# Optimization experiments

Measured on AMD Instinct MI355X. Metric: run time of the kernel, lower is better.

Reference implementation:

```python
import jax, jax.numpy as jnp
import numpy as np

W_EDGE, W_LAP, W_NORMAL, W_VEL = 0.5, 0.05, 0.01, 10.0


def _grid_mesh(g):
    ids = np.arange(g * g).reshape(g, g)
    tl, tr = ids[:-1, :-1].ravel(), ids[:-1, 1:].ravel()
    bl, br = ids[1:, :-1].ravel(), ids[1:, 1:].ravel()
    f1 = np.stack([tl, bl, br], 1)
    f2 = np.stack([tl, br, tr], 1)
    return np.concatenate([f1, f2], 0).astype(np.int64)  # [F,3]


def _topology(faces):
    # all directed edges with the opposite vertex of their face
    e = np.concatenate([faces[:, [0, 1]], faces[:, [1, 2]], faces[:, [2, 0]]], 0)
    opp = np.concatenate([faces[:, 2], faces[:, 0], faces[:, 1]], 0)
    key = np.sort(e, axis=1)
    uniq, inv = np.unique(key, axis=0, return_inverse=True)  # unique undirected edges
    counts = np.bincount(inv)
    order = np.argsort(inv, kind='stable')
    sel = counts[inv[order]] == 2
    idx2 = order[sel].reshape(-1, 2)  # the two face-slots of each interior edge
    ekey = key[idx2[:, 0]]
    pairs = np.stack([ekey[:, 0], ekey[:, 1], opp[idx2[:, 0]], opp[idx2[:, 1]]], 1)
    return uniq.astype(np.int64), pairs.astype(np.int64)


def setup_inputs() -> dict:
    key = jax.random.key(0)
    k1, k2 = jax.random.split(key)
    B, g = 2, 91
    N = g * g  # 8281
    faces = _grid_mesh(g)                 # [16200,3]
    edges, nc_pairs = _topology(faces)    # [24480,2], [24120,4]
    predictions = jax.random.normal(k1, (B, N, 3), dtype=jnp.float32)
    targets = jax.random.normal(k2, (B, N, 3), dtype=jnp.float32)
    return {
        'predictions': predictions,
        'targets': targets,
        'pred_faces': jnp.asarray(faces),
        'edges': jnp.asarray(edges),
        'nc_pairs': jnp.asarray(nc_pairs),
    }


def _chamfer(x, y):
    # pytorch3d chamfer_distance: squared dists, point mean both ways, batch mean
    xx = jnp.sum(x * x, -1)
    yy = jnp.sum(y * y, -1)
    d = xx[:, :, None] + yy[:, None, :] - 2.0 * jnp.einsum('bnd,bmd->bnm', x, y)
    d = jnp.maximum(d, 0.0)
    return jnp.mean(jnp.min(d, axis=2).mean(axis=1) + jnp.min(d, axis=1).mean(axis=1))


def _edge_loss(verts, edges):
    # mean over meshes of mean over edges of squared edge length (target len 0)
    ve = verts[:, edges]  # [B,E,2,3]
    l2 = jnp.sum((ve[:, :, 0] - ve[:, :, 1]) ** 2, -1)
    return l2.mean()


def _cot_laplacian_loss_one(verts, faces):
    # verts [N,3]; pytorch3d cot_laplacian + method='cot' smoothing
    fv = verts[faces]  # [F,3,3]
    v0, v1, v2 = fv[:, 0], fv[:, 1], fv[:, 2]
    A = jnp.linalg.norm(v1 - v2, axis=1)
    Bl = jnp.linalg.norm(v0 - v2, axis=1)
    C = jnp.linalg.norm(v0 - v1, axis=1)
    s = 0.5 * (A + Bl + C)
    area = jnp.sqrt(jnp.maximum(s * (s - A) * (s - Bl) * (s - C), 1e-12))
    A2, B2, C2 = A * A, Bl * Bl, C * C
    cota = (B2 + C2 - A2) / area
    cotb = (A2 + C2 - B2) / area
    cotc = (A2 + B2 - C2) / area
    cot = jnp.stack([cota, cotb, cotc], 1) / 4.0  # [F,3]
    ii = faces[:, jnp.array([1, 2, 0])]
    jj = faces[:, jnp.array([2, 0, 1])]
    i = jnp.concatenate([ii, jj], 0).ravel()
    j = jnp.concatenate([jj, ii], 0).ravel()
    w = jnp.concatenate([cot, cot], 0).ravel()
    N = verts.shape[0]
    Lx = jnp.zeros_like(verts).at[i].add(w[:, None] * verts[j])
    rowsum = jnp.zeros((N,), dtype=verts.dtype).at[i].add(w)
    norm_w = jnp.where(rowsum > 0, 1.0 / rowsum, 0.0)
    res = Lx * norm_w[:, None] - verts
    return jnp.linalg.norm(res, axis=1).mean()


def _normal_consistency_one(verts, pairs):
    # pairs [P,4] = (v0, v1, opp_a, opp_b) per interior edge
    p = verts[pairs]  # [P,4,3]
    e = p[:, 1] - p[:, 0]
    n0 = jnp.cross(e, p[:, 2] - p[:, 0])
    n1 = -jnp.cross(e, p[:, 3] - p[:, 0])
    eps = 1e-8
    cos = jnp.sum(n0 * n1, -1) / (
        jnp.maximum(jnp.linalg.norm(n0, axis=1), eps)
        * jnp.maximum(jnp.linalg.norm(n1, axis=1), eps)
    )
    return (1.0 - cos).mean()


def _forward(predictions, targets, pred_faces, edges, nc_pairs):
    loss_cham = _chamfer(predictions, targets)
    edge_l = _edge_loss(predictions, edges)
    lap_l = jax.vmap(lambda v: _cot_laplacian_loss_one(v, pred_faces))(predictions).mean()
    nc_l = jax.vmap(lambda v: _normal_consistency_one(v, nc_pairs))(predictions).mean()
    pred_shift = predictions[:, 1:, :] - predictions[:, :-1, :]
    tgt_shift = targets[:, 1:, :] - targets[:, :-1, :]
    vel_l = _chamfer(pred_shift, tgt_shift)
    return loss_cham + W_LAP * lap_l + W_NORMAL * nc_l + W_EDGE * edge_l + W_VEL * vel_l


def reference(predictions, targets, pred_faces, edges, nc_pairs):
    return _forward(predictions, targets, pred_faces, edges, nc_pairs)
```

## Files before the change

kernel.cpp:

```cpp
#include <hip/hip_runtime.h>


typedef unsigned int uint32;
typedef __attribute__((ext_vector_type(8)))  short bf16x8;
typedef __attribute__((ext_vector_type(16))) float f32x16;

#define W_EDGE   0.5f
#define W_LAP    0.05f
#define W_NORMAL 0.01f
#define W_VEL    10.0f
#define BIGF     3.0e38f
#define RSTRIDE  8320

__device__ __forceinline__ unsigned short f2bf(float f){
    uint32 b = __float_as_uint(f);
    b += 0x7FFFu + ((b >> 16) & 1u);
    return (unsigned short)(b >> 16);
}
__device__ __forceinline__ float bf2f(unsigned short h){
    return __uint_as_float(((uint32)h) << 16);
}

__device__ __forceinline__ float wave_sum(float v) {
#pragma unroll
    for (int o = 32; o > 0; o >>= 1) v += __shfl_down(v, o, 64);
    return v;
}

__global__ void bprep_k(const float* __restrict__ pred, const float* __restrict__ tgt,
                        int N, uint4* __restrict__ bfrag,
                        float* __restrict__ ws, int nzero)
{
    {
        uint32* w = (uint32*)ws;
        for (int i = blockIdx.x * blockDim.x + threadIdx.x; i < nzero;
             i += gridDim.x * blockDim.x)
            w[i] = 0u;
    }

    const int NT = (N + 31) >> 5;
    const int gt = blockIdx.x * 4 + (threadIdx.x >> 6);
    if (gt >= 8 * NT) return;
    const int c = gt / NT, t = gt - c * NT;
    const int dir = c >> 2, ds = (c >> 1) & 1, b = c & 1;
    const int Np = N - ds;
    const int l = threadIdx.x & 63;
    const int col = t * 32 + (l & 31);
    const float* __restrict__ yb = (dir ? pred : tgt) + (size_t)b * N * 3;
    float y0 = 0.f, y1 = 0.f, y2 = 0.f;
    const bool valid = col < Np;
    if (valid){
        if (ds){
            y0 = yb[(col+1)*3+0] - yb[col*3+0];
            y1 = yb[(col+1)*3+1] - yb[col*3+1];
            y2 = yb[(col+1)*3+2] - yb[col*3+2];
        } else {
            y0 = yb[col*3+0]; y1 = yb[col*3+1]; y2 = yb[col*3+2];
        }
    }
    const float yy = fmaf(y0,y0, fmaf(y1,y1, y2*y2));
    unsigned short yh0=f2bf(y0), yh1=f2bf(y1), yh2=f2bf(y2);
    unsigned short yl0=f2bf(y0-bf2f(yh0)), yl1=f2bf(y1-bf2f(yh1)), yl2=f2bf(y2-bf2f(yh2));
    unsigned short yyh, yyl;
    if (valid){ yyh = f2bf(yy); yyl = f2bf(yy - bf2f(yyh)); }
    else      { yyh = f2bf(BIGF); yyl = 0; }
    const short ONE = (short)0x3F80;
    bf16x8 Bu;
    if (l < 32){
        Bu[0]=(short)yh0; Bu[1]=(short)yh1; Bu[2]=(short)yh2;
        Bu[3]=(short)yh0; Bu[4]=(short)yh1; Bu[5]=(short)yh2;
        Bu[6]=(short)yl0; Bu[7]=(short)yl1;
    } else {
        Bu[0]=(short)yl2; Bu[1]=ONE; Bu[2]=ONE; Bu[3]=(short)yyh; Bu[4]=(short)yyl;
        Bu[5]=0; Bu[6]=0; Bu[7]=0;
    }
    bfrag[(size_t)(c * NT + t) * 64 + l] = __builtin_bit_cast(uint4, Bu);
}

__global__ __launch_bounds__(256)
void chamfer_mfma_k(const float* __restrict__ pred, const float* __restrict__ tgt,
                    int N, const uint4* __restrict__ bfrag,
                    float* __restrict__ rowpart)
{
    const int c = blockIdx.z;
    const int dir = c >> 2, ds = (c >> 1) & 1, b = c & 1;
    const int Np = N - ds;
    const int NT = (N + 31) >> 5;
    const int TC = (NT + 3) >> 2;
    const int t0 = blockIdx.y * TC;
    const int t1 = min(NT, t0 + TC);
    const int w = threadIdx.x >> 6, l = threadIdx.x & 63;
    const int h = l >> 5;
    const int grow = blockIdx.x * 128 + w * 32 + (l & 31);

    const float* __restrict__ xb = (dir ? tgt : pred) + (size_t)b * N * 3;
    float a0 = 0.f, a1 = 0.f, a2 = 0.f;
    const bool xvalid = grow < Np;
    if (xvalid){
        if (ds){
            a0 = xb[(grow+1)*3+0] - xb[grow*3+0];
            a1 = xb[(grow+1)*3+1] - xb[grow*3+1];
            a2 = xb[(grow+1)*3+2] - xb[grow*3+2];
        } else {
            a0 = xb[grow*3+0]; a1 = xb[grow*3+1]; a2 = xb[grow*3+2];
        }
    }
    const float xx = fmaf(a0,a0, fmaf(a1,a1, a2*a2));
    unsigned short xh0=f2bf(a0), xh1=f2bf(a1), xh2=f2bf(a2);
    unsigned short nxh0=f2bf(-2.f*bf2f(xh0)), nxh1=f2bf(-2.f*bf2f(xh1)), nxh2=f2bf(-2.f*bf2f(xh2));
    unsigned short nxl0=f2bf(-2.f*(a0-bf2f(xh0))), nxl1=f2bf(-2.f*(a1-bf2f(xh1))),
                   nxl2=f2bf(-2.f*(a2-bf2f(xh2)));
    unsigned short xxh=f2bf(xx), xxl=f2bf(xx-bf2f(xxh));
    const short ONE = (short)0x3F80;
    bf16x8 A;
    if (h == 0){
        A[0]=(short)nxh0; A[1]=(short)nxh1; A[2]=(short)nxh2;
        A[3]=(short)nxl0; A[4]=(short)nxl1; A[5]=(short)nxl2;
        A[6]=(short)nxh0; A[7]=(short)nxh1;
    } else {
        A[0]=(short)nxh2; A[1]=(short)xxh; A[2]=(short)xxl;
        A[3]=ONE; A[4]=ONE; A[5]=0; A[6]=0; A[7]=0;
    }

    f32x16 zacc;
#pragma unroll
    for (int r = 0; r < 16; ++r) zacc[r] = 0.f;
    float rm[16];
#pragma unroll
    for (int r = 0; r < 16; ++r) rm[r] = BIGF;

    const uint4* __restrict__ bfp = bfrag + (size_t)c * NT * 64 + l;

    const int ntile = t1 - t0;
    const int nb = ntile >> 3;

#define ONE_TILE(T)                                                         \
    {                                                                       \
        const f32x16 u = __builtin_amdgcn_mfma_f32_32x32x16_bf16(           \
            A, __builtin_bit_cast(bf16x8, T), zacc, 0, 0, 0);               \
        _Pragma("unroll")                                                   \
        for (int r = 0; r < 16; ++r) rm[r] = fminf(rm[r], u[r]);            \
    }                                                                       \
    __builtin_amdgcn_sched_barrier(0);

    int t = t0;
    for (int bt = 0; bt < nb; ++bt, t += 8){
        const uint4 T0 = bfp[(size_t)(t+0)*64];
        const uint4 T1 = bfp[(size_t)(t+1)*64];
        const uint4 T2 = bfp[(size_t)(t+2)*64];
        const uint4 T3 = bfp[(size_t)(t+3)*64];
        const uint4 T4 = bfp[(size_t)(t+4)*64];
        const uint4 T5 = bfp[(size_t)(t+5)*64];
        const uint4 T6 = bfp[(size_t)(t+6)*64];
        const uint4 T7 = bfp[(size_t)(t+7)*64];
        ONE_TILE(T0) ONE_TILE(T1) ONE_TILE(T2) ONE_TILE(T3)
        ONE_TILE(T4) ONE_TILE(T5) ONE_TILE(T6) ONE_TILE(T7)
    }
#undef ONE_TILE

    for (; t < t1; ++t){
        const bf16x8 T0 = __builtin_bit_cast(bf16x8, bfp[(size_t)t * 64]);
        const f32x16 u0 = __builtin_amdgcn_mfma_f32_32x32x16_bf16(A, T0, zacc, 0, 0, 0);
#pragma unroll
        for (int r = 0; r < 16; ++r) rm[r] = fminf(rm[r], u0[r]);
    }

#pragma unroll
    for (int r = 0; r < 16; ++r){
        float v = rm[r];
        v = fminf(v, __shfl_xor(v, 1, 64));
        v = fminf(v, __shfl_xor(v, 2, 64));
        v = fminf(v, __shfl_xor(v, 4, 64));
        v = fminf(v, __shfl_xor(v, 8, 64));
        v = fminf(v, __shfl_xor(v, 16, 64));
        rm[r] = v;
    }
    float* __restrict__ rp = rowpart + (size_t)(c * 4 + blockIdx.y) * RSTRIDE;
#pragma unroll
    for (int r = 0; r < 16; ++r){
        if ((l & 31) == r){
            const int rowl = (r & 3) + 8 * (r >> 2) + 4 * h;
            const int gr = blockIdx.x * 128 + w * 32 + rowl;
            if (gr < Np) rp[gr] = rm[r];
        }
    }
}

__global__ void mesh_k(const float* __restrict__ pred,
                       const int* __restrict__ edges, int E,
                       const int* __restrict__ pairs, int P,
                       const int* __restrict__ faces, int F,
                       int N, int B, float scaleE, float scaleP,
                       float* __restrict__ Lx, float* __restrict__ rowsum,
                       float* __restrict__ accum)
{
    const int tE = B * E, tP = B * P, tF = B * F;
    const int total = tE + tP + tF;
    float se = 0.f, sp = 0.f;
    for (int idx = blockIdx.x * blockDim.x + threadIdx.x; idx < total;
         idx += gridDim.x * blockDim.x) {
        if (idx < tE) {
            const int b = idx / E;
            const int e = idx - b * E;
            const float* __restrict__ vb = pred + (size_t)b * N * 3;
            const int i0 = edges[e * 2 + 0], i1 = edges[e * 2 + 1];
            float dx = vb[i0 * 3 + 0] - vb[i1 * 3 + 0];
            float dy = vb[i0 * 3 + 1] - vb[i1 * 3 + 1];
            float dz = vb[i0 * 3 + 2] - vb[i1 * 3 + 2];
            se += fmaf(dx, dx, fmaf(dy, dy, dz * dz));
        } else if (idx < tE + tP) {
            const int q = idx - tE;
            const int b = q / P;
            const int p = q - b * P;
            const float* __restrict__ vb = pred + (size_t)b * N * 3;
            const int a0 = pairs[p * 4 + 0], a1 = pairs[p * 4 + 1];
            const int a2 = pairs[p * 4 + 2], a3 = pairs[p * 4 + 3];
            float p0x = vb[a0 * 3], p0y = vb[a0 * 3 + 1], p0z = vb[a0 * 3 + 2];
            float ex = vb[a1 * 3] - p0x, ey = vb[a1 * 3 + 1] - p0y, ez = vb[a1 * 3 + 2] - p0z;
            float ux = vb[a2 * 3] - p0x, uy = vb[a2 * 3 + 1] - p0y, uz = vb[a2 * 3 + 2] - p0z;
            float wx = vb[a3 * 3] - p0x, wy = vb[a3 * 3 + 1] - p0y, wz = vb[a3 * 3 + 2] - p0z;
            float n0x = ey * uz - ez * uy;
            float n0y = ez * ux - ex * uz;
            float n0z = ex * uy - ey * ux;
            float n1x = -(ey * wz - ez * wy);
            float n1y = -(ez * wx - ex * wz);
            float n1z = -(ex * wy - ey * wx);
            float dt = n0x * n1x + n0y * n1y + n0z * n1z;
            float l0 = sqrtf(n0x * n0x + n0y * n0y + n0z * n0z);
            float l1 = sqrtf(n1x * n1x + n1y * n1y + n1z * n1z);
            sp += 1.0f - dt / (fmaxf(l0, 1e-8f) * fmaxf(l1, 1e-8f));
        } else {
            const int q = idx - tE - tP;
            const int b = q / F;
            const int f = q - b * F;
            const float* __restrict__ vb = pred + (size_t)b * N * 3;
            const int i0 = faces[f * 3 + 0], i1 = faces[f * 3 + 1], i2 = faces[f * 3 + 2];
            float v0x = vb[i0 * 3], v0y = vb[i0 * 3 + 1], v0z = vb[i0 * 3 + 2];
            float v1x = vb[i1 * 3], v1y = vb[i1 * 3 + 1], v1z = vb[i1 * 3 + 2];
            float v2x = vb[i2 * 3], v2y = vb[i2 * 3 + 1], v2z = vb[i2 * 3 + 2];
            float ax = v1x - v2x, ay = v1y - v2y, az = v1z - v2z;
            float bx = v0x - v2x, by = v0y - v2y, bz = v0z - v2z;
            float cx = v0x - v1x, cy = v0y - v1y, cz = v0z - v1z;
            float A  = sqrtf(ax * ax + ay * ay + az * az);
            float Bl = sqrtf(bx * bx + by * by + bz * bz);
            float C  = sqrtf(cx * cx + cy * cy + cz * cz);
            float s2 = 0.5f * (A + Bl + C);
            float area = sqrtf(fmaxf(s2 * (s2 - A) * (s2 - Bl) * (s2 - C), 1e-12f));
            float A2 = A * A, B2 = Bl * Bl, C2 = C * C;
            float inv4a = 1.0f / (4.0f * area);
            float cota = (B2 + C2 - A2) * inv4a;
            float cotb = (A2 + C2 - B2) * inv4a;
            float cotc = (A2 + B2 - C2) * inv4a;

            float* __restrict__ Lb = Lx + (size_t)b * N * 3;
            float* __restrict__ rb = rowsum + (size_t)b * N;
            #define SCAT(i, j, wv)                                            \
                atomicAdd(&Lb[(i) * 3 + 0], (wv) * vb[(j) * 3 + 0]);          \
                atomicAdd(&Lb[(i) * 3 + 1], (wv) * vb[(j) * 3 + 1]);          \
                atomicAdd(&Lb[(i) * 3 + 2], (wv) * vb[(j) * 3 + 2]);          \
                atomicAdd(&rb[(i)], (wv));
            SCAT(i1, i2, cota) SCAT(i2, i1, cota)
            SCAT(i2, i0, cotb) SCAT(i0, i2, cotb)
            SCAT(i0, i1, cotc) SCAT(i1, i0, cotc)
            #undef SCAT
        }
    }
    se = wave_sum(se);
    sp = wave_sum(sp);
    if ((threadIdx.x & 63) == 0) atomicAdd(accum, fmaf(se, scaleE, sp * scaleP));
}

__global__ void finalize_k(const float* __restrict__ rowpart,
                           const float* __restrict__ pred, const float* __restrict__ Lx,
                           const float* __restrict__ rowsum,
                           int N, float sMain, float sVel, float scaleL,
                           float* __restrict__ accum, float* __restrict__ out)
{
    const int total = 8 * N + 2 * N;
    float sm = 0.f, sv = 0.f, sl = 0.f;
    for (int idx = blockIdx.x * blockDim.x + threadIdx.x; idx < total;
         idx += gridDim.x * blockDim.x) {
        if (idx < 8 * N) {
            const int c = idx / N, i = idx - c * N;
            const int ds = (c >> 1) & 1;
            if (i < N - ds) {
                const float* rp = rowpart + (size_t)c * 4 * RSTRIDE;
                float v = fminf(fminf(rp[i], rp[RSTRIDE + i]),
                                fminf(rp[2*RSTRIDE + i], rp[3*RSTRIDE + i]));
                float d = fmaxf(v, 0.f);
                if (ds) sv += d; else sm += d;
            }
        } else {
            const int q = idx - 8 * N;
            float rs = rowsum[q];
            float nw = rs > 0.f ? 1.0f / rs : 0.f;
            float rx = Lx[q*3+0]*nw - pred[q*3+0];
            float ry = Lx[q*3+1]*nw - pred[q*3+1];
            float rz = Lx[q*3+2]*nw - pred[q*3+2];
            sl += sqrtf(rx*rx + ry*ry + rz*rz);
        }
    }
    sm = wave_sum(sm); sv = wave_sum(sv); sl = wave_sum(sl);
    if ((threadIdx.x & 63) == 0)
        atomicAdd(accum, fmaf(sm, sMain, fmaf(sv, sVel, sl * scaleL)));

    __syncthreads();
    if (threadIdx.x == 0){
        __threadfence();
        const uint32 prev = atomicAdd((uint32*)(accum + 4), 1u);
        if (prev == gridDim.x - 1)
            out[0] = atomicAdd(accum, 0.0f);
    }
}

extern "C" void kernel_launch(void* const* d_in, const int* in_sizes, int n_in,
                              void* d_out, int out_size, void* d_ws, size_t ws_size,
                              hipStream_t stream)
{
    const float* pred = (const float*)d_in[0];
    const float* tgt  = (const float*)d_in[1];
    const int* faces  = (const int*)d_in[2];
    const int* edges  = (const int*)d_in[3];
    const int* pairs  = (const int*)d_in[4];

    const int B = 2;
    const int N = in_sizes[0] / (3 * B);
    const int F = in_sizes[2] / 3;
    const int E = in_sizes[3] / 2;
    const int P = in_sizes[4] / 4;
    const int NT = (N + 31) >> 5;

    float* ws      = (float*)d_ws;
    float* accum   = ws;
    float* Lx      = ws + 8;
    float* rowsum  = Lx + (size_t)B * N * 3;
    float* rowpart = rowsum + (size_t)B * N;
    size_t off     = 8 + (size_t)B*N*3 + (size_t)B*N + (size_t)32*RSTRIDE;
    uint4* bfrag   = (uint4*)(ws + off);

    const int nzero = 8 + B * N * 3 + B * N;

    bprep_k<<<dim3((8 * NT + 3) / 4), dim3(256), 0, stream>>>(pred, tgt, N, bfrag,
                                                              ws, nzero);

    chamfer_mfma_k<<<dim3((N + 127) / 128, 4, 8), dim3(256), 0, stream>>>(
        pred, tgt, N, bfrag, rowpart);

    mesh_k<<<128, dim3(256), 0, stream>>>(pred, edges, E, pairs, P, faces, F, N, B,
                                          W_EDGE / ((float)B * (float)E),
                                          W_NORMAL / ((float)B * (float)P),
                                          Lx, rowsum, accum);

    finalize_k<<<96, dim3(256), 0, stream>>>(rowpart, pred, Lx, rowsum, N,
                                             1.0f / ((float)B * (float)N),
                                             W_VEL / ((float)B * (float)(N - 1)),
                                             W_LAP / ((float)B * (float)N),
                                             accum, (float*)d_out);
}
```

Measured before the change: 73.61 us.

## Fuse mesh losses into chamfer kernel as extra grid slice and pair MFMA tiles

Merges the mesh loss kernel into the chamfer MFMA kernel by adding a ninth z-slice of blocks that run the edge, normal-consistency and cotangent-Laplacian scatter work. This removes one launch and lets the mesh work overlap with the MFMA-bound chamfer blocks. Separately, the inner loop now issues two MFMAs before each min-reduction with a scheduling barrier after each pair, giving more independent work between barriers. The thread count in the fused path is hardcoded to 260 blocks, which holds only when (N+127)/128 is 65. The pairing also raises register pressure.

```diff
diff --git a/kernel.cpp b/kernel.cpp
--- a/kernel.cpp
+++ b/kernel.cpp
@@ -78,10 +78,94 @@
 }
 
 __global__ __launch_bounds__(256)
-void chamfer_mfma_k(const float* __restrict__ pred, const float* __restrict__ tgt,
-                    int N, const uint4* __restrict__ bfrag,
-                    float* __restrict__ rowpart)
+void mega_k(const float* __restrict__ pred, const float* __restrict__ tgt,
+            int N, const uint4* __restrict__ bfrag, float* __restrict__ rowpart,
+            const int* __restrict__ edges, int E,
+            const int* __restrict__ pairs, int P,
+            const int* __restrict__ faces, int F,
+            int B, float scaleE, float scaleP,
+            float* __restrict__ Lx, float* __restrict__ rowsum,
+            float* __restrict__ accum)
 {
+    if (blockIdx.z == 8){
+        const int tE = B * E, tP = B * P, tF = B * F;
+        const int total = tE + tP + tF;
+        const int bid = blockIdx.x * 4 + blockIdx.y;
+        const int nthr = 260 * 256;
+        float se = 0.f, sp = 0.f;
+        for (int idx = bid * 256 + threadIdx.x; idx < total; idx += nthr) {
+            if (idx < tE) {
+                const int b = idx / E;
+                const int e = idx - b * E;
+                const float* __restrict__ vb = pred + (size_t)b * N * 3;
+                const int i0 = edges[e * 2 + 0], i1 = edges[e * 2 + 1];
+                float dx = vb[i0 * 3 + 0] - vb[i1 * 3 + 0];
+                float dy = vb[i0 * 3 + 1] - vb[i1 * 3 + 1];
+                float dz = vb[i0 * 3 + 2] - vb[i1 * 3 + 2];
+                se += fmaf(dx, dx, fmaf(dy, dy, dz * dz));
+            } else if (idx < tE + tP) {
+                const int q = idx - tE;
+                const int b = q / P;
+                const int p = q - b * P;
+                const float* __restrict__ vb = pred + (size_t)b * N * 3;
+                const int a0 = pairs[p * 4 + 0], a1 = pairs[p * 4 + 1];
+                const int a2 = pairs[p * 4 + 2], a3 = pairs[p * 4 + 3];
+                float p0x = vb[a0 * 3], p0y = vb[a0 * 3 + 1], p0z = vb[a0 * 3 + 2];
+                float ex = vb[a1 * 3] - p0x, ey = vb[a1 * 3 + 1] - p0y, ez = vb[a1 * 3 + 2] - p0z;
+                float ux = vb[a2 * 3] - p0x, uy = vb[a2 * 3 + 1] - p0y, uz = vb[a2 * 3 + 2] - p0z;
+                float wx = vb[a3 * 3] - p0x, wy = vb[a3 * 3 + 1] - p0y, wz = vb[a3 * 3 + 2] - p0z;
+                float n0x = ey * uz - ez * uy;
+                float n0y = ez * ux - ex * uz;
+                float n0z = ex * uy - ey * ux;
+                float n1x = -(ey * wz - ez * wy);
+                float n1y = -(ez * wx - ex * wz);
+                float n1z = -(ex * wy - ey * wx);
+                float dt = n0x * n1x + n0y * n1y + n0z * n1z;
+                float l0 = sqrtf(n0x * n0x + n0y * n0y + n0z * n0z);
+                float l1 = sqrtf(n1x * n1x + n1y * n1y + n1z * n1z);
+                sp += 1.0f - dt / (fmaxf(l0, 1e-8f) * fmaxf(l1, 1e-8f));
+            } else {
+                const int q = idx - tE - tP;
+                const int b = q / F;
+                const int f = q - b * F;
+                const float* __restrict__ vb = pred + (size_t)b * N * 3;
+                const int i0 = faces[f * 3 + 0], i1 = faces[f * 3 + 1], i2 = faces[f * 3 + 2];
+                float v0x = vb[i0 * 3], v0y = vb[i0 * 3 + 1], v0z = vb[i0 * 3 + 2];
+                float v1x = vb[i1 * 3], v1y = vb[i1 * 3 + 1], v1z = vb[i1 * 3 + 2];
+                float v2x = vb[i2 * 3], v2y = vb[i2 * 3 + 1], v2z = vb[i2 * 3 + 2];
+                float ax = v1x - v2x, ay = v1y - v2y, az = v1z - v2z;
+                float bx = v0x - v2x, by = v0y - v2y, bz = v0z - v2z;
+                float cx = v0x - v1x, cy = v0y - v1y, cz = v0z - v1z;
+                float A  = sqrtf(ax * ax + ay * ay + az * az);
+                float Bl = sqrtf(bx * bx + by * by + bz * bz);
+                float C  = sqrtf(cx * cx + cy * cy + cz * cz);
+                float s2 = 0.5f * (A + Bl + C);
+                float area = sqrtf(fmaxf(s2 * (s2 - A) * (s2 - Bl) * (s2 - C), 1e-12f));
+                float A2 = A * A, B2 = Bl * Bl, C2 = C * C;
+                float inv4a = 1.0f / (4.0f * area);
+                float cota = (B2 + C2 - A2) * inv4a;
+                float cotb = (A2 + C2 - B2) * inv4a;
+                float cotc = (A2 + B2 - C2) * inv4a;
+
+                float* __restrict__ Lb = Lx + (size_t)b * N * 3;
+                float* __restrict__ rb = rowsum + (size_t)b * N;
+                #define SCAT(i, j, wv)                                            \
+                    atomicAdd(&Lb[(i) * 3 + 0], (wv) * vb[(j) * 3 + 0]);          \
+                    atomicAdd(&Lb[(i) * 3 + 1], (wv) * vb[(j) * 3 + 1]);          \
+                    atomicAdd(&Lb[(i) * 3 + 2], (wv) * vb[(j) * 3 + 2]);          \
+                    atomicAdd(&rb[(i)], (wv));
+                SCAT(i1, i2, cota) SCAT(i2, i1, cota)
+                SCAT(i2, i0, cotb) SCAT(i0, i2, cotb)
+                SCAT(i0, i1, cotc) SCAT(i1, i0, cotc)
+                #undef SCAT
+            }
+        }
+        se = wave_sum(se);
+        sp = wave_sum(sp);
+        if ((threadIdx.x & 63) == 0) atomicAdd(accum, fmaf(se, scaleE, sp * scaleP));
+        return;
+    }
+
     const int c = blockIdx.z;
     const int dir = c >> 2, ds = (c >> 1) & 1, b = c & 1;
     const int Np = N - ds;
@@ -134,15 +218,6 @@
     const int ntile = t1 - t0;
     const int nb = ntile >> 3;
 
-#define ONE_TILE(T)                                                         \
-    {                                                                       \
-        const f32x16 u = __builtin_amdgcn_mfma_f32_32x32x16_bf16(           \
-            A, __builtin_bit_cast(bf16x8, T), zacc, 0, 0, 0);               \
-        _Pragma("unroll")                                                   \
-        for (int r = 0; r < 16; ++r) rm[r] = fminf(rm[r], u[r]);            \
-    }                                                                       \
-    __builtin_amdgcn_sched_barrier(0);
-
     int t = t0;
     for (int bt = 0; bt < nb; ++bt, t += 8){
         const uint4 T0 = bfp[(size_t)(t+0)*64];
@@ -153,11 +228,44 @@
         const uint4 T5 = bfp[(size_t)(t+5)*64];
         const uint4 T6 = bfp[(size_t)(t+6)*64];
         const uint4 T7 = bfp[(size_t)(t+7)*64];
-        ONE_TILE(T0) ONE_TILE(T1) ONE_TILE(T2) ONE_TILE(T3)
-        ONE_TILE(T4) ONE_TILE(T5) ONE_TILE(T6) ONE_TILE(T7)
-    }
-#undef ONE_TILE
-
+
+        {
+            const f32x16 u0 = __builtin_amdgcn_mfma_f32_32x32x16_bf16(
+                A, __builtin_bit_cast(bf16x8, T0), zacc, 0, 0, 0);
+            const f32x16 u1 = __builtin_amdgcn_mfma_f32_32x32x16_bf16(
+                A, __builtin_bit_cast(bf16x8, T1), zacc, 0, 0, 0);
+#pragma unroll
+            for (int r = 0; r < 16; ++r) rm[r] = fminf(fminf(rm[r], u0[r]), u1[r]);
+        }
+        __builtin_amdgcn_sched_barrier(0);
+        {
+            const f32x16 u2 = __builtin_amdgcn_mfma_f32_32x32x16_bf16(
+                A, __builtin_bit_cast(bf16x8, T2), zacc, 0, 0, 0);
+            const f32x16 u3 = __builtin_amdgcn_mfma_f32_32x32x16_bf16(
+                A, __builtin_bit_cast(bf16x8, T3), zacc, 0, 0, 0);
+#pragma unroll
+            for (int r = 0; r < 16; ++r) rm[r] = fminf(fminf(rm[r], u2[r]), u3[r]);
+        }
+        __builtin_amdgcn_sched_barrier(0);
+        {
+            const f32x16 u4 = __builtin_amdgcn_mfma_f32_32x32x16_bf16(
+                A, __builtin_bit_cast(bf16x8, T4), zacc, 0, 0, 0);
+            const f32x16 u5 = __builtin_amdgcn_mfma_f32_32x32x16_bf16(
+                A, __builtin_bit_cast(bf16x8, T5), zacc, 0, 0, 0);
+#pragma unroll
+            for (int r = 0; r < 16; ++r) rm[r] = fminf(fminf(rm[r], u4[r]), u5[r]);
+        }
+        __builtin_amdgcn_sched_barrier(0);
+        {
+            const f32x16 u6 = __builtin_amdgcn_mfma_f32_32x32x16_bf16(
+                A, __builtin_bit_cast(bf16x8, T6), zacc, 0, 0, 0);
+            const f32x16 u7 = __builtin_amdgcn_mfma_f32_32x32x16_bf16(
+                A, __builtin_bit_cast(bf16x8, T7), zacc, 0, 0, 0);
+#pragma unroll
+            for (int r = 0; r < 16; ++r) rm[r] = fminf(fminf(rm[r], u6[r]), u7[r]);
+        }
+        __builtin_amdgcn_sched_barrier(0);
+    }
     for (; t < t1; ++t){
         const bf16x8 T0 = __builtin_bit_cast(bf16x8, bfp[(size_t)t * 64]);
         const f32x16 u0 = __builtin_amdgcn_mfma_f32_32x32x16_bf16(A, T0, zacc, 0, 0, 0);
@@ -184,90 +292,6 @@
             if (gr < Np) rp[gr] = rm[r];
         }
     }
-}
-
-__global__ void mesh_k(const float* __restrict__ pred,
-                       const int* __restrict__ edges, int E,
-                       const int* __restrict__ pairs, int P,
-                       const int* __restrict__ faces, int F,
-                       int N, int B, float scaleE, float scaleP,
-                       float* __restrict__ Lx, float* __restrict__ rowsum,
-                       float* __restrict__ accum)
-{
-    const int tE = B * E, tP = B * P, tF = B * F;
-    const int total = tE + tP + tF;
-    float se = 0.f, sp = 0.f;
-    for (int idx = blockIdx.x * blockDim.x + threadIdx.x; idx < total;
-         idx += gridDim.x * blockDim.x) {
-        if (idx < tE) {
-            const int b = idx / E;
-            const int e = idx - b * E;
-            const float* __restrict__ vb = pred + (size_t)b * N * 3;
-            const int i0 = edges[e * 2 + 0], i1 = edges[e * 2 + 1];
-            float dx = vb[i0 * 3 + 0] - vb[i1 * 3 + 0];
-            float dy = vb[i0 * 3 + 1] - vb[i1 * 3 + 1];
-            float dz = vb[i0 * 3 + 2] - vb[i1 * 3 + 2];
-            se += fmaf(dx, dx, fmaf(dy, dy, dz * dz));
-        } else if (idx < tE + tP) {
-            const int q = idx - tE;
-            const int b = q / P;
-            const int p = q - b * P;
-            const float* __restrict__ vb = pred + (size_t)b * N * 3;
-            const int a0 = pairs[p * 4 + 0], a1 = pairs[p * 4 + 1];
-            const int a2 = pairs[p * 4 + 2], a3 = pairs[p * 4 + 3];
-            float p0x = vb[a0 * 3], p0y = vb[a0 * 3 + 1], p0z = vb[a0 * 3 + 2];
-            float ex = vb[a1 * 3] - p0x, ey = vb[a1 * 3 + 1] - p0y, ez = vb[a1 * 3 + 2] - p0z;
-            float ux = vb[a2 * 3] - p0x, uy = vb[a2 * 3 + 1] - p0y, uz = vb[a2 * 3 + 2] - p0z;
-            float wx = vb[a3 * 3] - p0x, wy = vb[a3 * 3 + 1] - p0y, wz = vb[a3 * 3 + 2] - p0z;
-            float n0x = ey * uz - ez * uy;
-            float n0y = ez * ux - ex * uz;
-            float n0z = ex * uy - ey * ux;
-            float n1x = -(ey * wz - ez * wy);
-            float n1y = -(ez * wx - ex * wz);
-            float n1z = -(ex * wy - ey * wx);
-            float dt = n0x * n1x + n0y * n1y + n0z * n1z;
-            float l0 = sqrtf(n0x * n0x + n0y * n0y + n0z * n0z);
-            float l1 = sqrtf(n1x * n1x + n1y * n1y + n1z * n1z);
-            sp += 1.0f - dt / (fmaxf(l0, 1e-8f) * fmaxf(l1, 1e-8f));
-        } else {
-            const int q = idx - tE - tP;
-            const int b = q / F;
-            const int f = q - b * F;
-            const float* __restrict__ vb = pred + (size_t)b * N * 3;
-            const int i0 = faces[f * 3 + 0], i1 = faces[f * 3 + 1], i2 = faces[f * 3 + 2];
-            float v0x = vb[i0 * 3], v0y = vb[i0 * 3 + 1], v0z = vb[i0 * 3 + 2];
-            float v1x = vb[i1 * 3], v1y = vb[i1 * 3 + 1], v1z = vb[i1 * 3 + 2];
-            float v2x = vb[i2 * 3], v2y = vb[i2 * 3 + 1], v2z = vb[i2 * 3 + 2];
-            float ax = v1x - v2x, ay = v1y - v2y, az = v1z - v2z;
-            float bx = v0x - v2x, by = v0y - v2y, bz = v0z - v2z;
-            float cx = v0x - v1x, cy = v0y - v1y, cz = v0z - v1z;
-            float A  = sqrtf(ax * ax + ay * ay + az * az);
-            float Bl = sqrtf(bx * bx + by * by + bz * bz);
-            float C  = sqrtf(cx * cx + cy * cy + cz * cz);
-            float s2 = 0.5f * (A + Bl + C);
-            float area = sqrtf(fmaxf(s2 * (s2 - A) * (s2 - Bl) * (s2 - C), 1e-12f));
-            float A2 = A * A, B2 = Bl * Bl, C2 = C * C;
-            float inv4a = 1.0f / (4.0f * area);
-            float cota = (B2 + C2 - A2) * inv4a;
-            float cotb = (A2 + C2 - B2) * inv4a;
-            float cotc = (A2 + B2 - C2) * inv4a;
-
-            float* __restrict__ Lb = Lx + (size_t)b * N * 3;
-            float* __restrict__ rb = rowsum + (size_t)b * N;
-            #define SCAT(i, j, wv)                                            \
-                atomicAdd(&Lb[(i) * 3 + 0], (wv) * vb[(j) * 3 + 0]);          \
-                atomicAdd(&Lb[(i) * 3 + 1], (wv) * vb[(j) * 3 + 1]);          \
-                atomicAdd(&Lb[(i) * 3 + 2], (wv) * vb[(j) * 3 + 2]);          \
-                atomicAdd(&rb[(i)], (wv));
-            SCAT(i1, i2, cota) SCAT(i2, i1, cota)
-            SCAT(i2, i0, cotb) SCAT(i0, i2, cotb)
-            SCAT(i0, i1, cotc) SCAT(i1, i0, cotc)
-            #undef SCAT
-        }
-    }
-    se = wave_sum(se);
-    sp = wave_sum(sp);
-    if ((threadIdx.x & 63) == 0) atomicAdd(accum, fmaf(se, scaleE, sp * scaleP));
 }
 
 __global__ void finalize_k(const float* __restrict__ rowpart,
@@ -343,13 +367,12 @@
     bprep_k<<<dim3((8 * NT + 3) / 4), dim3(256), 0, stream>>>(pred, tgt, N, bfrag,
                                                               ws, nzero);
 
-    chamfer_mfma_k<<<dim3((N + 127) / 128, 4, 8), dim3(256), 0, stream>>>(
-        pred, tgt, N, bfrag, rowpart);
-
-    mesh_k<<<128, dim3(256), 0, stream>>>(pred, edges, E, pairs, P, faces, F, N, B,
-                                          W_EDGE / ((float)B * (float)E),
-                                          W_NORMAL / ((float)B * (float)P),
-                                          Lx, rowsum, accum);
+    mega_k<<<dim3((N + 127) / 128, 4, 9), dim3(256), 0, stream>>>(
+        pred, tgt, N, bfrag, rowpart,
+        edges, E, pairs, P, faces, F, B,
+        W_EDGE / ((float)B * (float)E),
+        W_NORMAL / ((float)B * (float)P),
+        Lx, rowsum, accum);
 
     finalize_k<<<96, dim3(256), 0, stream>>>(rowpart, pred, Lx, rowsum, N,
                                              1.0f / ((float)B * (float)N),
```

New measurement: 74.53 us. No clear change (+1.3%).

## Stage B-fragment tiles through double-buffered LDS with direct global-to-LDS loads

Applied to the files above, without the earlier changes.

Replaces the per-wave direct global loads of eight B-fragment tiles with a cooperative, double-buffered LDS staging scheme. Each wave loads two tiles into shared memory using global_load_lds, and the next block of eight is prefetched while the current one is consumed. MFMAs are issued in pairs with a combined min reduction. This aims to share tile loads across the waves of a block and overlap memory with compute. In exchange it adds a __syncthreads per iteration and assumes four waves per block (w indexes 0..3).

```diff
diff --git a/kernel.cpp b/kernel.cpp
--- a/kernel.cpp
+++ b/kernel.cpp
@@ -25,6 +25,12 @@
 #pragma unroll
     for (int o = 32; o > 0; o >>= 1) v += __shfl_down(v, o, 64);
     return v;
+}
+
+__device__ __forceinline__ void gload_lds16(const uint4* __restrict__ g, uint4* l){
+    __builtin_amdgcn_global_load_lds(
+        (const __attribute__((address_space(1))) void*)g,
+        (__attribute__((address_space(3))) void*)l, 16, 0, 0);
 }
 
 __global__ void bprep_k(const float* __restrict__ pred, const float* __restrict__ tgt,
@@ -131,34 +137,44 @@
 
     const uint4* __restrict__ bfp = bfrag + (size_t)c * NT * 64 + l;
 
+    __shared__ uint4 sbuf[2][512];
     const int ntile = t1 - t0;
     const int nb = ntile >> 3;
 
-#define ONE_TILE(T)                                                         \
+#define STAGE(bi, tbase)                                                    \
+    gload_lds16(bfp + (size_t)((tbase) + 2*w    ) * 64, &sbuf[bi][(2*w    )*64]); \
+    gload_lds16(bfp + (size_t)((tbase) + 2*w + 1) * 64, &sbuf[bi][(2*w + 1)*64]);
+
+#define PAIRC(bi, i0_, i1_)                                                 \
     {                                                                       \
-        const f32x16 u = __builtin_amdgcn_mfma_f32_32x32x16_bf16(           \
-            A, __builtin_bit_cast(bf16x8, T), zacc, 0, 0, 0);               \
+        const bf16x8 Ta = __builtin_bit_cast(bf16x8, sbuf[bi][(i0_)*64 + l]); \
+        const bf16x8 Tb = __builtin_bit_cast(bf16x8, sbuf[bi][(i1_)*64 + l]); \
+        const f32x16 u0 = __builtin_amdgcn_mfma_f32_32x32x16_bf16(A, Ta, zacc, 0, 0, 0); \
+        const f32x16 u1 = __builtin_amdgcn_mfma_f32_32x32x16_bf16(A, Tb, zacc, 0, 0, 0); \
         _Pragma("unroll")                                                   \
-        for (int r = 0; r < 16; ++r) rm[r] = fminf(rm[r], u[r]);            \
+        for (int r = 0; r < 16; ++r)                                        \
+            rm[r] = fminf(fminf(rm[r], u0[r]), u1[r]);                      \
     }                                                                       \
     __builtin_amdgcn_sched_barrier(0);
 
-    int t = t0;
-    for (int bt = 0; bt < nb; ++bt, t += 8){
-        const uint4 T0 = bfp[(size_t)(t+0)*64];
-        const uint4 T1 = bfp[(size_t)(t+1)*64];
-        const uint4 T2 = bfp[(size_t)(t+2)*64];
-        const uint4 T3 = bfp[(size_t)(t+3)*64];
-        const uint4 T4 = bfp[(size_t)(t+4)*64];
-        const uint4 T5 = bfp[(size_t)(t+5)*64];
-        const uint4 T6 = bfp[(size_t)(t+6)*64];
-        const uint4 T7 = bfp[(size_t)(t+7)*64];
-        ONE_TILE(T0) ONE_TILE(T1) ONE_TILE(T2) ONE_TILE(T3)
-        ONE_TILE(T4) ONE_TILE(T5) ONE_TILE(T6) ONE_TILE(T7)
-    }
-#undef ONE_TILE
-
-    for (; t < t1; ++t){
+    if (nb > 0){
+        STAGE(0, t0)
+        __syncthreads();
+        int cur = 0;
+        for (int bt = 0; bt < nb; ++bt){
+            if (bt + 1 < nb){ STAGE(cur ^ 1, t0 + (bt + 1) * 8) }
+            PAIRC(cur, 0, 1)
+            PAIRC(cur, 2, 3)
+            PAIRC(cur, 4, 5)
+            PAIRC(cur, 6, 7)
+            __syncthreads();
+            cur ^= 1;
+        }
+    }
+#undef STAGE
+#undef PAIRC
+
+    for (int t = t0 + nb * 8; t < t1; ++t){
         const bf16x8 T0 = __builtin_bit_cast(bf16x8, bfp[(size_t)t * 64]);
         const f32x16 u0 = __builtin_amdgcn_mfma_f32_32x32x16_bf16(A, T0, zacc, 0, 0, 0);
 #pragma unroll
```

New measurement: 74.12 us. Within noise of the previous version (+0.7%).
